# Performance work log

Hardware: AMD Instinct MI355X
Metric: run time of the kernel (lower is better)

Reference implementation:

```python
import jax, jax.numpy as jnp
import numpy as np

D_MODEL = 1024
NHEAD = 16
HEAD_DIM = D_MODEL // NHEAD
D_FF = 4096
EPS = 1e-8


def rmsnorm(x, w):
    # matches torch: norm = ||x||_2 / sqrt(d); out = w * x / (rms + eps)
    rms = jnp.linalg.norm(x, axis=-1, keepdims=True) / np.sqrt(x.shape[-1])
    return w * (x / (rms + EPS))


def setup_inputs() -> dict:
    key = jax.random.key(0)
    ks = jax.random.split(key, 11)
    B, S = 4, 2048
    init = lambda k, shape, fan_in: jax.random.uniform(k, shape, jnp.float32, -1.0, 1.0) / np.sqrt(fan_in)
    return {
        "src": jax.random.normal(ks[0], (B, S, D_MODEL), jnp.float32),
        "qkv_w": init(ks[1], (D_MODEL, 3 * D_MODEL), D_MODEL),
        "qkv_b": init(ks[2], (3 * D_MODEL,), D_MODEL),
        "out_w": init(ks[3], (D_MODEL, D_MODEL), D_MODEL),
        "out_b": init(ks[4], (D_MODEL,), D_MODEL),
        "ff1_w": init(ks[5], (D_MODEL, D_FF), D_MODEL),
        "ff1_b": init(ks[6], (D_FF,), D_MODEL),
        "ff2_w": init(ks[7], (D_FF, D_MODEL), D_FF),
        "ff2_b": init(ks[8], (D_MODEL,), D_FF),
        "norm1_w": jnp.ones((D_MODEL,), jnp.float32),
        "norm2_w": jnp.ones((D_MODEL,), jnp.float32),
    }


def reference(src, qkv_w, qkv_b, out_w, out_b, ff1_w, ff1_b, ff2_w, ff2_b, norm1_w, norm2_w):
    B, S, _ = src.shape
    # --- pre-norm attention block ---
    x = rmsnorm(src, norm1_w)
    qkv = x @ qkv_w + qkv_b                     # [B,S,3*D]
    qkv = qkv.reshape(B, S, 3, NHEAD, HEAD_DIM)
    q, k, v = qkv[:, :, 0], qkv[:, :, 1], qkv[:, :, 2]   # [B,S,H,D]
    scores = jnp.einsum('bshd,bthd->bhst', q, k) / np.sqrt(HEAD_DIM)
    attn = jax.nn.softmax(scores, axis=-1)
    ctx = jnp.einsum('bhst,bthd->bshd', attn, v).reshape(B, S, D_MODEL)
    src = src + ctx @ out_w + out_b
    # --- pre-norm FFN block ---
    y = rmsnorm(src, norm2_w)
    h = jax.nn.gelu(y @ ff1_w + ff1_b, approximate=False)
    src = src + h @ ff2_w + ff2_b
    return src
```

## Files before the change

### kernel.cpp

```cpp
#include <hip/hip_runtime.h>
#include <hip/hip_bf16.h>

#define DM   1024
#define DFF  4096
#define NH   16
#define HD   64
#define SEQ  2048
#define BATCH 4
#define NTOK (BATCH*SEQ)

typedef float  f32x4  __attribute__((ext_vector_type(4)));
typedef short  bf16x8 __attribute__((ext_vector_type(8)));

#define SBAR() asm volatile("s_barrier" ::: "memory")
#define S_VMCNT(N) asm volatile("s_waitcnt vmcnt(" #N ")" ::: "memory")

__device__ __forceinline__ unsigned short f2bf(float f) {
    unsigned int x = __builtin_bit_cast(unsigned int, f);
    x += 0x7fff + ((x >> 16) & 1);
    return (unsigned short)(x >> 16);
}
__device__ __forceinline__ float bf2f(unsigned short u) {
    unsigned int x = (unsigned int)u << 16;
    return __builtin_bit_cast(float, x);
}

__device__ __forceinline__ float fexp2(float x) {
    float r; asm("v_exp_f32 %0, %1" : "=v"(r) : "v"(x)); return r;
}
__device__ __forceinline__ float frcp(float x) {
    float r; asm("v_rcp_f32 %0, %1" : "=v"(r) : "v"(x)); return r;
}

__device__ __forceinline__ void gload_lds16(const void* g, void* l) {
    __builtin_amdgcn_global_load_lds(
        (const __attribute__((address_space(1))) unsigned int*)g,
        (__attribute__((address_space(3))) unsigned int*)l,
        16, 0, 0);
}

__device__ __forceinline__ int swz(int row, int elem) { return elem ^ ((row & 7) << 3); }

__global__ __launch_bounds__(256)
void convT_all(const float* __restrict__ qkv_w, const float* __restrict__ out_w,
               const float* __restrict__ ff1_w, const float* __restrict__ ff2_w,
               unsigned short* __restrict__ qkv_wt, unsigned short* __restrict__ out_wt,
               unsigned short* __restrict__ ff1_wt, unsigned short* __restrict__ ff2_wt)
{
    __shared__ float tile[32][33];
    const float* W; unsigned short* Wt; int K, N, bx, by;
    int b = blockIdx.x;
    if (b < 3072)      { W = qkv_w; Wt = qkv_wt; K = 1024; N = 3072; bx = b % 96;  by = b / 96;  }
    else if (b < 4096) { int i = b - 3072; W = out_w; Wt = out_wt; K = 1024; N = 1024; bx = i % 32;  by = i / 32; }
    else if (b < 8192) { int i = b - 4096; W = ff1_w; Wt = ff1_wt; K = 1024; N = 4096; bx = i % 128; by = i / 128; }
    else               { int i = b - 8192; W = ff2_w; Wt = ff2_wt; K = 4096; N = 1024; bx = i % 32;  by = i / 32; }
    int n0 = bx * 32, k0 = by * 32;
    int tx = threadIdx.x & 31, ty = threadIdx.x >> 5;
    #pragma unroll
    for (int i = 0; i < 4; ++i)
        tile[ty + i*8][tx] = W[(size_t)(k0 + ty + i*8) * N + n0 + tx];
    __syncthreads();
    #pragma unroll
    for (int i = 0; i < 4; ++i)
        Wt[(size_t)(n0 + ty + i*8) * K + k0 + tx] = f2bf(tile[tx][ty + i*8]);
}

template<bool BF16IN>
__global__ __launch_bounds__(256)
void rmsnorm_kernel(const void* __restrict__ inp, const float* __restrict__ w,
                    unsigned short* __restrict__ out)
{
    __shared__ float red[4];
    int row = blockIdx.x, t = threadIdx.x;
    float x0, x1, x2, x3;
    if constexpr (BF16IN) {
        ushort4 u = ((const ushort4*)((const unsigned short*)inp + (size_t)row * DM))[t];
        x0 = bf2f(u.x); x1 = bf2f(u.y); x2 = bf2f(u.z); x3 = bf2f(u.w);
    } else {
        float4 v = ((const float4*)((const float*)inp + (size_t)row * DM))[t];
        x0 = v.x; x1 = v.y; x2 = v.z; x3 = v.w;
    }
    float ss = x0*x0 + x1*x1 + x2*x2 + x3*x3;
    #pragma unroll
    for (int m = 1; m < 64; m <<= 1) ss += __shfl_xor(ss, m);
    if ((t & 63) == 0) red[t >> 6] = ss;
    __syncthreads();
    float tot = red[0] + red[1] + red[2] + red[3];
    float rms = sqrtf(tot) * (1.f / 32.f);
    float inv = 1.f / (rms + 1e-8f);
    float4 wv = ((const float4*)w)[t];
    unsigned int lo = (unsigned int)f2bf(x0*inv*wv.x) | ((unsigned int)f2bf(x1*inv*wv.y) << 16);
    unsigned int hi = (unsigned int)f2bf(x2*inv*wv.z) | ((unsigned int)f2bf(x3*inv*wv.w) << 16);
    uint2 pk; pk.x = lo; pk.y = hi;
    *(uint2*)(out + (size_t)row * DM + t * 4) = pk;
}

template<int MODE, int NB>
__global__ __launch_bounds__(512, 2)
void gemm_tpl(const unsigned short* __restrict__ A,
              const unsigned short* __restrict__ Bt,
              const float* __restrict__ bias,
              int N, int K, int nx,
              const float* __restrict__ residf,
              const unsigned short* __restrict__ residb,
              float* __restrict__ outf,
              unsigned short* __restrict__ outb,
              unsigned short* __restrict__ q,
              unsigned short* __restrict__ kk,
              unsigned short* __restrict__ vt)
{
    constexpr int NJ = NB / 64;
    constexpr int WN = NB / 4;
    __shared__ __align__(16) unsigned short Atile[2][2][256 * 32];
    __shared__ __align__(16) unsigned short Btile[2][2][NB * 32];
    const int tid = threadIdx.x, w = tid >> 6, l = tid & 63;
    const int lr = l & 15, lh = l >> 4;
    const int wm = w >> 2, wn = w & 3;
    const int nwg = gridDim.x, cpx = nwg >> 3;
    const int sid = (blockIdx.x & 7) * cpx + (blockIdx.x >> 3);
    const int by = sid / nx, bx = sid - by * nx;
    const int m0 = by * 256, n0 = bx * NB;
    const int nkt = K >> 6;
    const int srow = w * 16 + (l >> 2);
    const int scol = (((l & 3) ^ (srow & 3)) << 3);

    auto stageA = [&](int kt, int ks, int half, int bi) {
        int r0 = half * 128;
        gload_lds16(A + (size_t)(m0 + r0 + srow) * K + kt * 64 + ks * 32 + scol,
                    &Atile[bi][ks][(r0 + w * 16) * 32]);
    };
    auto stageB = [&](int kt, int ks, int half, int bi) {
        int r0 = half * 128;
        gload_lds16(Bt + (size_t)(n0 + r0 + srow) * K + kt * 64 + ks * 32 + scol,
                    &Btile[bi][ks][(r0 + w * 16) * 32]);
    };

    f32x4 acc[8][NJ];
    #pragma unroll
    for (int a = 0; a < 8; ++a)
        #pragma unroll
        for (int j = 0; j < NJ; ++j) acc[a][j] = {0.f, 0.f, 0.f, 0.f};

    #pragma unroll
    for (int ks = 0; ks < 2; ++ks) {
        stageA(0, ks, 0, 0); stageA(0, ks, 1, 0);
        stageB(0, ks, 0, 0);
        if (NB == 256) stageB(0, ks, 1, 0);
    }

    int bi = 0;
    for (int t = 0; t < nkt; ++t) {
        #pragma unroll
        for (int ks = 0; ks < 2; ++ks) {
            if (ks == 0 || t + 1 < nkt) {
                if constexpr (NB == 256) { S_VMCNT(4); } else { S_VMCNT(3); }
            } else {
                S_VMCNT(0);
            }
            SBAR();
            bf16x8 bB[NJ];
            #pragma unroll
            for (int j = 0; j < NJ; ++j) {
                int row = wn * WN + j * 16 + lr;
                bB[j] = *(const bf16x8*)&Btile[bi][ks][row * 32 + ((lh ^ (row & 3)) << 3)];
            }
            #pragma unroll
            for (int rho = 0; rho < 2; ++rho) {
                bf16x8 aA[4];
                #pragma unroll
                for (int i = 0; i < 4; ++i) {
                    int row = wm * 128 + rho * 64 + i * 16 + lr;
                    aA[i] = *(const bf16x8*)&Atile[bi][ks][row * 32 + ((lh ^ (row & 3)) << 3)];
                }
                if (t + 1 < nkt) {
                    if (rho == 0) { stageA(t + 1, ks, 0, bi ^ 1); stageA(t + 1, ks, 1, bi ^ 1); }
                    else          { stageB(t + 1, ks, 0, bi ^ 1);
                                    if (NB == 256) stageB(t + 1, ks, 1, bi ^ 1); }
                }
                SBAR();
                __builtin_amdgcn_s_setprio(1);
                #pragma unroll
                for (int i = 0; i < 4; ++i)
                    #pragma unroll
                    for (int j = 0; j < NJ; ++j)
                        acc[rho * 4 + i][j] = __builtin_amdgcn_mfma_f32_16x16x32_bf16(
                            aA[i], bB[j], acc[rho * 4 + i][j], 0, 0, 0);
                __builtin_amdgcn_s_setprio(0);
            }
        }
        bi ^= 1;
    }

    #pragma unroll
    for (int a = 0; a < 8; ++a) {
        const int rho = a >> 2, i = a & 3;
        #pragma unroll
        for (int j = 0; j < NJ; ++j) {
            const int col = n0 + wn * WN + j * 16 + lr;
            const int row0 = m0 + wm * 128 + rho * 64 + i * 16 + lh * 4;
            if (MODE == 0) {
                float v0 = acc[a][j][0] + bias[col];
                float v1 = acc[a][j][1] + bias[col];
                float v2 = acc[a][j][2] + bias[col];
                float v3 = acc[a][j][3] + bias[col];
                int wh = col >> 10, h = (col >> 6) & 15, d = col & 63;
                int b = row0 >> 11, s0 = row0 & 2047;
                size_t base = (size_t)(b * NH + h);
                if (wh == 0) {
                    q[(base * SEQ + s0    ) * HD + d] = f2bf(v0 * 0.18033688f);
                    q[(base * SEQ + s0 + 1) * HD + d] = f2bf(v1 * 0.18033688f);
                    q[(base * SEQ + s0 + 2) * HD + d] = f2bf(v2 * 0.18033688f);
                    q[(base * SEQ + s0 + 3) * HD + d] = f2bf(v3 * 0.18033688f);
                } else if (wh == 1) {
                    kk[(base * SEQ + s0    ) * HD + d] = f2bf(v0);
                    kk[(base * SEQ + s0 + 1) * HD + d] = f2bf(v1);
                    kk[(base * SEQ + s0 + 2) * HD + d] = f2bf(v2);
                    kk[(base * SEQ + s0 + 3) * HD + d] = f2bf(v3);
                } else {
                    uint2 pk;
                    pk.x = (unsigned int)f2bf(v0) | ((unsigned int)f2bf(v1) << 16);
                    pk.y = (unsigned int)f2bf(v2) | ((unsigned int)f2bf(v3) << 16);
                    *(uint2*)&vt[(base * HD + d) * SEQ + s0] = pk;
                }
            } else {
                #pragma unroll
                for (int r = 0; r < 4; ++r) {
                    int row = row0 + r;
                    float v = acc[a][j][r] + bias[col];
                    if (MODE == 2) {
                        float x = v;
                        float t2 = fmaf(x * x * x, 0.044715f, x);
                        float av = fminf(t2 * 2.3022079f, 80.f);
                        float u = fexp2(av);
                        float g = x * u * frcp(u + 1.f);
                        outb[(size_t)row * N + col] = f2bf(g);
                    } else if (MODE == 3) {
                        outf[(size_t)row * N + col] = v + bf2f(residb[(size_t)row * N + col]);
                    } else {
                        outb[(size_t)row * N + col] = f2bf(v + residf[(size_t)row * N + col]);
                    }
                }
            }
        }
    }
}

__global__ __launch_bounds__(256, 2)
void attn_kernel(const unsigned short* __restrict__ q,
                 const unsigned short* __restrict__ k,
                 const unsigned short* __restrict__ vt,
                 unsigned short* __restrict__ ctx)
{
    __shared__ __align__(16) unsigned short Ks[2][64 * 64];
    __shared__ __align__(16) unsigned short Vs[2][64 * 64];
    __shared__ __align__(16) unsigned short PQ[4][64 * 64];

    const int tid = threadIdx.x, w = tid >> 6, l = tid & 63;
    const int lr = l & 15, lh = l >> 4;

    const int sid = (blockIdx.x & 7) * 64 + (blockIdx.x >> 3);
    const int bh = sid >> 3, qt = sid & 7;
    const int b = bh >> 4, h = bh & 15;

    const int rloc = l >> 3;
    const int cswz = (((l & 7) ^ rloc) << 3);

    const unsigned short* kbase0 = k  + (size_t)bh * SEQ * HD;
    const unsigned short* vbase0 = vt + (size_t)bh * HD * SEQ;
    const int NT = SEQ / 64;

    auto stageK = [&](int t, int buf) {
        const unsigned short* kb = kbase0 + (size_t)t * 64 * HD;
        #pragma unroll
        for (int c = 0; c < 2; ++c) {
            int r0 = (w * 2 + c) * 8;
            gload_lds16(kb + (size_t)(r0 + rloc) * HD + cswz, &Ks[buf][r0 * 64]);
        }
    };
    auto stageV = [&](int t, int buf) {
        const unsigned short* vb = vbase0 + t * 64;
        #pragma unroll
        for (int c = 0; c < 2; ++c) {
            int d0 = w * 16 + c * 8;
            gload_lds16(vb + (size_t)(d0 + rloc) * SEQ + cswz, &Vs[buf][d0 * 64]);
        }
    };

    unsigned short* Pw = &PQ[w][0];
    const unsigned short* qbase = q + ((size_t)bh * SEQ + qt * 256 + w * 64) * HD;
    #pragma unroll
    for (int c = 0; c < 8; ++c) {
        int r0 = c * 8;
        gload_lds16(qbase + (size_t)(r0 + rloc) * HD + cswz, &Pw[r0 * 64]);
    }
    stageK(0, 0);
    stageV(0, 0);
    S_VMCNT(4);
    bf16x8 aq[4][2];
    #pragma unroll
    for (int g = 0; g < 4; ++g) {
        int row = g * 16 + lr;
        aq[g][0] = *(const bf16x8*)&Pw[row * 64 + swz(row,      lh * 8)];
        aq[g][1] = *(const bf16x8*)&Pw[row * 64 + swz(row, 32 + lh * 8)];
    }
    __syncthreads();

    bf16x8 vone;
    #pragma unroll
    for (int i = 0; i < 8; ++i) vone[i] = (short)0x3F80;

    f32x4 lacc[4];
    f32x4 o[4][4];
    #pragma unroll
    for (int g = 0; g < 4; ++g) {
        lacc[g] = {0.f, 0.f, 0.f, 0.f};
        #pragma unroll
        for (int nf = 0; nf < 4; ++nf) o[g][nf] = {0.f, 0.f, 0.f, 0.f};
    }

    for (int t = 0; t < NT; ++t) {
        const int cur = t & 1;
        if (t + 1 < NT) { stageK(t + 1, cur ^ 1); stageV(t + 1, cur ^ 1); }

        const unsigned short* Kc = &Ks[cur][0];
        const unsigned short* Vc = &Vs[cur][0];

        bf16x8 kb[4][2];
        #pragma unroll
        for (int j = 0; j < 4; ++j) {
            int kr = j * 16 + lr;
            kb[j][0] = *(const bf16x8*)&Kc[kr * 64 + swz(kr,      lh * 8)];
            kb[j][1] = *(const bf16x8*)&Kc[kr * 64 + swz(kr, 32 + lh * 8)];
        }

        #pragma unroll
        for (int g = 0; g < 4; ++g) {
            f32x4 sc[4];
            __builtin_amdgcn_s_setprio(1);
            #pragma unroll
            for (int j = 0; j < 4; ++j) {
                f32x4 z = {0.f, 0.f, 0.f, 0.f};
                z = __builtin_amdgcn_mfma_f32_16x16x32_bf16(kb[j][0], aq[g][0], z, 0, 0, 0);
                z = __builtin_amdgcn_mfma_f32_16x16x32_bf16(kb[j][1], aq[g][1], z, 0, 0, 0);
                sc[j] = z;
            }
            __builtin_amdgcn_s_setprio(0);

            int prow = g * 16 + lr;
            #pragma unroll
            for (int j = 0; j < 4; ++j) {
                float p0 = fexp2(sc[j][0]), p1 = fexp2(sc[j][1]);
                float p2 = fexp2(sc[j][2]), p3 = fexp2(sc[j][3]);
                unsigned int w0, w1;
                asm("v_cvt_pk_bf16_f32 %0, %1, %2" : "=v"(w0) : "v"(p0), "v"(p1));
                asm("v_cvt_pk_bf16_f32 %0, %1, %2" : "=v"(w1) : "v"(p2), "v"(p3));
                int k0 = j * 16 + lh * 4;
                int e = prow * 64 + (k0 ^ ((prow & 7) << 3));
                uint2 pk; pk.x = w0; pk.y = w1;
                *(uint2*)&Pw[e] = pk;
            }
        }

        bf16x8 ap[4][2];
        #pragma unroll
        for (int g = 0; g < 4; ++g) {
            int prow = g * 16 + lr;
            ap[g][0] = *(const bf16x8*)&Pw[prow * 64 + swz(prow,      lh * 8)];
            ap[g][1] = *(const bf16x8*)&Pw[prow * 64 + swz(prow, 32 + lh * 8)];
        }
        __builtin_amdgcn_s_setprio(1);
        #pragma unroll
        for (int g = 0; g < 4; ++g) {
            lacc[g] = __builtin_amdgcn_mfma_f32_16x16x32_bf16(ap[g][0], vone, lacc[g], 0, 0, 0);
            lacc[g] = __builtin_amdgcn_mfma_f32_16x16x32_bf16(ap[g][1], vone, lacc[g], 0, 0, 0);
        }
        #pragma unroll
        for (int nf = 0; nf < 4; ++nf) {
            int vr = nf * 16 + lr;
            bf16x8 vb0 = *(const bf16x8*)&Vc[vr * 64 + swz(vr,      lh * 8)];
            bf16x8 vb1 = *(const bf16x8*)&Vc[vr * 64 + swz(vr, 32 + lh * 8)];
            #pragma unroll
            for (int g = 0; g < 4; ++g) {
                o[g][nf] = __builtin_amdgcn_mfma_f32_16x16x32_bf16(ap[g][0], vb0, o[g][nf], 0, 0, 0);
                o[g][nf] = __builtin_amdgcn_mfma_f32_16x16x32_bf16(ap[g][1], vb1, o[g][nf], 0, 0, 0);
            }
        }
        __builtin_amdgcn_s_setprio(0);

        __syncthreads();
    }

    #pragma unroll
    for (int g = 0; g < 4; ++g) {
        float linv[4];
        #pragma unroll
        for (int r = 0; r < 4; ++r) linv[r] = frcp(lacc[g][r]);
        #pragma unroll
        for (int nf = 0; nf < 4; ++nf)
            #pragma unroll
            for (int r = 0; r < 4; ++r) {
                int row = qt * 256 + w * 64 + g * 16 + lh * 4 + r;
                ctx[((size_t)b * SEQ + row) * DM + h * 64 + nf * 16 + lr] =
                    f2bf(o[g][nf][r] * linv[r]);
            }
    }
}

extern "C" void kernel_launch(void* const* d_in, const int* in_sizes, int n_in,
                              void* d_out, int out_size, void* d_ws, size_t ws_size,
                              hipStream_t stream)
{
    const float* src   = (const float*)d_in[0];
    const float* qkv_w = (const float*)d_in[1];
    const float* qkv_b = (const float*)d_in[2];
    const float* out_w = (const float*)d_in[3];
    const float* out_b = (const float*)d_in[4];
    const float* ff1_w = (const float*)d_in[5];
    const float* ff1_b = (const float*)d_in[6];
    const float* ff2_w = (const float*)d_in[7];
    const float* ff2_b = (const float*)d_in[8];
    const float* n1_w  = (const float*)d_in[9];
    const float* n2_w  = (const float*)d_in[10];

    char* ws = (char*)d_ws;
    const size_t MB = 1u << 20;
    unsigned short* qkv_wt = (unsigned short*)(ws);
    unsigned short* out_wt = (unsigned short*)(ws + 6*MB);
    unsigned short* ff1_wt = (unsigned short*)(ws + 8*MB);
    unsigned short* ff2_wt = (unsigned short*)(ws + 16*MB);
    unsigned short* xb     = (unsigned short*)(ws + 24*MB);
    unsigned short* qb     = (unsigned short*)(ws + 40*MB);
    unsigned short* kb     = (unsigned short*)(ws + 56*MB);
    unsigned short* vtb    = (unsigned short*)(ws + 72*MB);
    unsigned short* hb     = (unsigned short*)(ws + 24*MB);
    unsigned short* ctxb   = (unsigned short*)(ws + 88*MB);
    unsigned short* yb     = (unsigned short*)(ws + 88*MB);
    unsigned short* src2b  = (unsigned short*)(ws + 104*MB);
    float* outp = (float*)d_out;

    convT_all<<<12288, 256, 0, stream>>>(qkv_w, out_w, ff1_w, ff2_w,
                                         qkv_wt, out_wt, ff1_wt, ff2_wt);

    rmsnorm_kernel<false><<<NTOK, 256, 0, stream>>>(src, n1_w, xb);

    gemm_tpl<0, 256><<<384, 512, 0, stream>>>(xb, qkv_wt, qkv_b, 3072, 1024, 12,
                                              nullptr, nullptr, nullptr, nullptr, qb, kb, vtb);

    attn_kernel<<<SEQ/256 * BATCH*NH, 256, 0, stream>>>(qb, kb, vtb, ctxb);

    gemm_tpl<4, 128><<<256, 512, 0, stream>>>(ctxb, out_wt, out_b, 1024, 1024, 8,
                                              src, nullptr, nullptr, src2b, nullptr, nullptr, nullptr);

    rmsnorm_kernel<true><<<NTOK, 256, 0, stream>>>(src2b, n2_w, yb);

    gemm_tpl<2, 256><<<512, 512, 0, stream>>>(yb, ff1_wt, ff1_b, 4096, 1024, 16,
                                              nullptr, nullptr, nullptr, hb, nullptr, nullptr, nullptr);

    gemm_tpl<3, 128><<<256, 512, 0, stream>>>(hb, ff2_wt, ff2_b, 1024, 4096, 8,
                                              nullptr, src2b, outp, nullptr, nullptr, nullptr, nullptr);
}
```

Before: 378.0 us.

## Merge weight prep with first RMSNorm and add dedicated 128x128 FF2 GEMM

Folds the first RMSNorm into the weight transpose/convert kernel as extra blocks, removing one launch and letting the two run concurrently. Replaces the FF2 GEMM (K=4096, N=1024) with a simpler 128x128-tile, 256-thread kernel launched with 512 blocks instead of 256, to improve CU occupancy on the small-N output. The new kernel is single-buffered, has no swizzle and syncs twice per k-step, so it may lose the overlap and LDS bank-conflict avoidance the templated GEMM had.

```diff
diff --git a/kernel.cpp b/kernel.cpp
--- a/kernel.cpp
+++ b/kernel.cpp
@@ -42,44 +42,57 @@
 __device__ __forceinline__ int swz(int row, int elem) { return elem ^ ((row & 7) << 3); }
 
 __global__ __launch_bounds__(256)
-void convT_all(const float* __restrict__ qkv_w, const float* __restrict__ out_w,
-               const float* __restrict__ ff1_w, const float* __restrict__ ff2_w,
-               unsigned short* __restrict__ qkv_wt, unsigned short* __restrict__ out_wt,
-               unsigned short* __restrict__ ff1_wt, unsigned short* __restrict__ ff2_wt)
+void prep_all(const float* __restrict__ qkv_w, const float* __restrict__ out_w,
+              const float* __restrict__ ff1_w, const float* __restrict__ ff2_w,
+              unsigned short* __restrict__ qkv_wt, unsigned short* __restrict__ out_wt,
+              unsigned short* __restrict__ ff1_wt, unsigned short* __restrict__ ff2_wt,
+              const float* __restrict__ src, const float* __restrict__ n1_w,
+              unsigned short* __restrict__ xb)
 {
     __shared__ float tile[32][33];
-    const float* W; unsigned short* Wt; int K, N, bx, by;
     int b = blockIdx.x;
-    if (b < 3072)      { W = qkv_w; Wt = qkv_wt; K = 1024; N = 3072; bx = b % 96;  by = b / 96;  }
-    else if (b < 4096) { int i = b - 3072; W = out_w; Wt = out_wt; K = 1024; N = 1024; bx = i % 32;  by = i / 32; }
-    else if (b < 8192) { int i = b - 4096; W = ff1_w; Wt = ff1_wt; K = 1024; N = 4096; bx = i % 128; by = i / 128; }
-    else               { int i = b - 8192; W = ff2_w; Wt = ff2_wt; K = 4096; N = 1024; bx = i % 32;  by = i / 32; }
-    int n0 = bx * 32, k0 = by * 32;
-    int tx = threadIdx.x & 31, ty = threadIdx.x >> 5;
-    #pragma unroll
-    for (int i = 0; i < 4; ++i)
-        tile[ty + i*8][tx] = W[(size_t)(k0 + ty + i*8) * N + n0 + tx];
-    __syncthreads();
-    #pragma unroll
-    for (int i = 0; i < 4; ++i)
-        Wt[(size_t)(n0 + ty + i*8) * K + k0 + tx] = f2bf(tile[tx][ty + i*8]);
-}
-
-template<bool BF16IN>
+    if (b < 12288) {
+        const float* W; unsigned short* Wt; int K, N, bx, by;
+        if (b < 3072)      { W = qkv_w; Wt = qkv_wt; K = 1024; N = 3072; bx = b % 96;  by = b / 96;  }
+        else if (b < 4096) { int i = b - 3072; W = out_w; Wt = out_wt; K = 1024; N = 1024; bx = i % 32;  by = i / 32; }
+        else if (b < 8192) { int i = b - 4096; W = ff1_w; Wt = ff1_wt; K = 1024; N = 4096; bx = i % 128; by = i / 128; }
+        else               { int i = b - 8192; W = ff2_w; Wt = ff2_wt; K = 4096; N = 1024; bx = i % 32;  by = i / 32; }
+        int n0 = bx * 32, k0 = by * 32;
+        int tx = threadIdx.x & 31, ty = threadIdx.x >> 5;
+        #pragma unroll
+        for (int i = 0; i < 4; ++i)
+            tile[ty + i*8][tx] = W[(size_t)(k0 + ty + i*8) * N + n0 + tx];
+        __syncthreads();
+        #pragma unroll
+        for (int i = 0; i < 4; ++i)
+            Wt[(size_t)(n0 + ty + i*8) * K + k0 + tx] = f2bf(tile[tx][ty + i*8]);
+    } else {
+        int row = b - 12288, t = threadIdx.x;
+        float4 v = ((const float4*)(src + (size_t)row * DM))[t];
+        float ss = v.x*v.x + v.y*v.y + v.z*v.z + v.w*v.w;
+        #pragma unroll
+        for (int m = 1; m < 64; m <<= 1) ss += __shfl_xor(ss, m);
+        if ((t & 63) == 0) tile[0][t >> 6] = ss;
+        __syncthreads();
+        float tot = tile[0][0] + tile[0][1] + tile[0][2] + tile[0][3];
+        float rms = sqrtf(tot) * (1.f / 32.f);
+        float inv = 1.f / (rms + 1e-8f);
+        float4 wv = ((const float4*)n1_w)[t];
+        unsigned int lo = (unsigned int)f2bf(v.x*inv*wv.x) | ((unsigned int)f2bf(v.y*inv*wv.y) << 16);
+        unsigned int hi = (unsigned int)f2bf(v.z*inv*wv.z) | ((unsigned int)f2bf(v.w*inv*wv.w) << 16);
+        uint2 pk; pk.x = lo; pk.y = hi;
+        *(uint2*)(xb + (size_t)row * DM + t * 4) = pk;
+    }
+}
+
 __global__ __launch_bounds__(256)
-void rmsnorm_kernel(const void* __restrict__ inp, const float* __restrict__ w,
+void rmsnorm_kernel(const unsigned short* __restrict__ inp, const float* __restrict__ w,
                     unsigned short* __restrict__ out)
 {
     __shared__ float red[4];
     int row = blockIdx.x, t = threadIdx.x;
-    float x0, x1, x2, x3;
-    if constexpr (BF16IN) {
-        ushort4 u = ((const ushort4*)((const unsigned short*)inp + (size_t)row * DM))[t];
-        x0 = bf2f(u.x); x1 = bf2f(u.y); x2 = bf2f(u.z); x3 = bf2f(u.w);
-    } else {
-        float4 v = ((const float4*)((const float*)inp + (size_t)row * DM))[t];
-        x0 = v.x; x1 = v.y; x2 = v.z; x3 = v.w;
-    }
+    ushort4 u = ((const ushort4*)(inp + (size_t)row * DM))[t];
+    float x0 = bf2f(u.x), x1 = bf2f(u.y), x2 = bf2f(u.z), x3 = bf2f(u.w);
     float ss = x0*x0 + x1*x1 + x2*x2 + x3*x3;
     #pragma unroll
     for (int m = 1; m < 64; m <<= 1) ss += __shfl_xor(ss, m);
@@ -102,7 +115,6 @@
               const float* __restrict__ bias,
               int N, int K, int nx,
               const float* __restrict__ residf,
-              const unsigned short* __restrict__ residb,
               float* __restrict__ outf,
               unsigned short* __restrict__ outb,
               unsigned short* __restrict__ q,
@@ -234,8 +246,6 @@
                         float u = fexp2(av);
                         float g = x * u * frcp(u + 1.f);
                         outb[(size_t)row * N + col] = f2bf(g);
-                    } else if (MODE == 3) {
-                        outf[(size_t)row * N + col] = v + bf2f(residb[(size_t)row * N + col]);
                     } else {
                         outb[(size_t)row * N + col] = f2bf(v + residf[(size_t)row * N + col]);
                     }
@@ -243,6 +253,73 @@
             }
         }
     }
+}
+
+__global__ __launch_bounds__(256)
+void gemm_ff2(const unsigned short* __restrict__ A,
+              const unsigned short* __restrict__ Bt,
+              const float* __restrict__ bias,
+              int N, int K, int nx,
+              const unsigned short* __restrict__ residb,
+              float* __restrict__ outf)
+{
+    __shared__ __align__(16) unsigned short As[128 * 64];
+    __shared__ __align__(16) unsigned short Bs[128 * 64];
+    const int tid = threadIdx.x;
+    const int w = tid >> 6, l = tid & 63;
+    const int lr = l & 15, lh = l >> 4;
+    const int nwg = gridDim.x, cpx = nwg >> 3;
+    const int sid = (blockIdx.x & 7) * cpx + (blockIdx.x >> 3);
+    const int by = sid / nx, bx = sid - by * nx;
+    const int m0 = by * 128, n0 = bx * 128;
+    const int wr = (w >> 1) * 64, wc = (w & 1) * 64;
+
+    f32x4 acc[4][4];
+    #pragma unroll
+    for (int i = 0; i < 4; ++i)
+        #pragma unroll
+        for (int j = 0; j < 4; ++j) acc[i][j] = {0.f, 0.f, 0.f, 0.f};
+
+    const int nkt = K >> 6;
+    for (int kt = 0; kt < nkt; ++kt) {
+        __syncthreads();
+        #pragma unroll
+        for (int c = 0; c < 4; ++c) {
+            int rbase = w * 32 + c * 8;
+            int row = rbase + (l >> 3);
+            int col = (l & 7) * 8;
+            gload_lds16(A  + (size_t)(m0 + row) * K + kt * 64 + col, &As[rbase * 64]);
+            gload_lds16(Bt + (size_t)(n0 + row) * K + kt * 64 + col, &Bs[rbase * 64]);
+        }
+        __syncthreads();
+        #pragma unroll
+        for (int ks = 0; ks < 2; ++ks) {
+            bf16x8 af[4], bfv[4];
+            #pragma unroll
+            for (int i = 0; i < 4; ++i)
+                af[i] = *(const bf16x8*)&As[(wr + i*16 + lr) * 64 + ks*32 + lh*8];
+            #pragma unroll
+            for (int j = 0; j < 4; ++j)
+                bfv[j] = *(const bf16x8*)&Bs[(wc + j*16 + lr) * 64 + ks*32 + lh*8];
+            #pragma unroll
+            for (int i = 0; i < 4; ++i)
+                #pragma unroll
+                for (int j = 0; j < 4; ++j)
+                    acc[i][j] = __builtin_amdgcn_mfma_f32_16x16x32_bf16(af[i], bfv[j], acc[i][j], 0, 0, 0);
+        }
+    }
+
+    #pragma unroll
+    for (int i = 0; i < 4; ++i)
+        #pragma unroll
+        for (int j = 0; j < 4; ++j)
+            #pragma unroll
+            for (int r = 0; r < 4; ++r) {
+                int row = m0 + wr + i*16 + lh*4 + r;
+                int col = n0 + wc + j*16 + lr;
+                float v = acc[i][j][r] + bias[col];
+                outf[(size_t)row * N + col] = v + bf2f(residb[(size_t)row * N + col]);
+            }
 }
 
 __global__ __launch_bounds__(256, 2)
@@ -438,24 +515,22 @@
     unsigned short* src2b  = (unsigned short*)(ws + 104*MB);
     float* outp = (float*)d_out;
 
-    convT_all<<<12288, 256, 0, stream>>>(qkv_w, out_w, ff1_w, ff2_w,
-                                         qkv_wt, out_wt, ff1_wt, ff2_wt);
-
-    rmsnorm_kernel<false><<<NTOK, 256, 0, stream>>>(src, n1_w, xb);
+    prep_all<<<12288 + NTOK, 256, 0, stream>>>(qkv_w, out_w, ff1_w, ff2_w,
+                                               qkv_wt, out_wt, ff1_wt, ff2_wt,
+                                               src, n1_w, xb);
 
     gemm_tpl<0, 256><<<384, 512, 0, stream>>>(xb, qkv_wt, qkv_b, 3072, 1024, 12,
-                                              nullptr, nullptr, nullptr, nullptr, qb, kb, vtb);
+                                              nullptr, nullptr, nullptr, qb, kb, vtb);
 
     attn_kernel<<<SEQ/256 * BATCH*NH, 256, 0, stream>>>(qb, kb, vtb, ctxb);
 
     gemm_tpl<4, 128><<<256, 512, 0, stream>>>(ctxb, out_wt, out_b, 1024, 1024, 8,
-                                              src, nullptr, nullptr, src2b, nullptr, nullptr, nullptr);
-
-    rmsnorm_kernel<true><<<NTOK, 256, 0, stream>>>(src2b, n2_w, yb);
+                                              src, nullptr, src2b, nullptr, nullptr, nullptr);
+
+    rmsnorm_kernel<<<NTOK, 256, 0, stream>>>(src2b, n2_w, yb);
 
     gemm_tpl<2, 256><<<512, 512, 0, stream>>>(yb, ff1_wt, ff1_b, 4096, 1024, 16,
-                                              nullptr, nullptr, nullptr, hb, nullptr, nullptr, nullptr);
-
-    gemm_tpl<3, 128><<<256, 512, 0, stream>>>(hb, ff2_wt, ff2_b, 1024, 4096, 8,
-                                              nullptr, src2b, outp, nullptr, nullptr, nullptr, nullptr);
-}
+                                              nullptr, nullptr, hb, nullptr, nullptr, nullptr);
+
+    gemm_ff2<<<512, 256, 0, stream>>>(hb, ff2_wt, ff2_b, 1024, 4096, 8, src2b, outp);
+}
```

Result: slower. 389.2 us (+3.0%).
